# Kernel optimization log

Hardware: AMD Instinct MI355X
Metric: run time of the kernel (lower is better)

## Reference

```python
import jax, jax.numpy as jnp
import numpy as np
from itertools import product

GRID_N = 256
N_RAYS, N_SAMPLES = 2048, 128


def setup_inputs() -> dict:
    key = jax.random.key(0)
    k1, k2 = jax.random.split(key)
    sdf_grid = jax.random.normal(k1, (GRID_N, GRID_N, GRID_N), dtype=jnp.float32)
    # monotone voxel-center coordinates over [-1, 1] (sdf_util.get_grid_pts analog)
    x_grid = jnp.linspace(-1.0, 1.0, GRID_N, dtype=jnp.float32)
    y_grid = jnp.linspace(-1.0, 1.0, GRID_N, dtype=jnp.float32)
    z_grid = jnp.linspace(-1.0, 1.0, GRID_N, dtype=jnp.float32)
    # single object pose (sdf_map_pose); identity as in SDFModel.__init__
    pose = jnp.eye(4, dtype=jnp.float32)
    # query sample points in [-0.95, 0.95]^3
    pts = jax.random.uniform(k2, (N_RAYS, N_SAMPLES, 3), dtype=jnp.float32,
                             minval=-0.95, maxval=0.95)
    return {"sdf_grid": sdf_grid, "x_grid": x_grid, "y_grid": y_grid,
            "z_grid": z_grid, "pose": pose, "pts": pts}


def _interp_axis(p, x):
    """Per-dim bucketize + left/right distances (torch.bucketize right=False
    == searchsorted side='left'). p: [N] sorted, x: [K]. Returns idx_l, idx_r,
    dist_l, dist_r, overall, all shape [K]."""
    n = p.shape[0]
    idx_r = jnp.searchsorted(p, x, side="left")
    idx_r = jnp.where(idx_r >= n, n - 1, idx_r)
    idx_l = jnp.clip(idx_r - 1, 0, n - 1)
    dist_l = jnp.maximum(x - p[idx_l], 0.0)
    dist_r = jnp.maximum(p[idx_r] - x, 0.0)
    both_zero = (dist_l == 0.0) & (dist_r == 0.0)
    dist_l = jnp.where(both_zero, 1.0, dist_l)
    dist_r = jnp.where(both_zero, 1.0, dist_r)
    return idx_l, idx_r, dist_l, dist_r, dist_l + dist_r


def reference(sdf_grid, x_grid, y_grid, z_grid, pose, pts):
    # SDFModel.transform with a single pose: x_obj = T_inv @ [x; 1]
    x = pts.reshape(-1, 3)                               # [K, 3]
    T_inv = jnp.linalg.inv(pose)
    x_obj = x @ T_inv[:3, :3].T + T_inv[:3, 3]           # [K, 3]

    grids = (x_grid, y_grid, z_grid)
    axis_data = [_interp_axis(p, x_obj[:, d]) for d, p in enumerate(grids)]
    idxs = [(a[0], a[1]) for a in axis_data]
    dists = [(a[2], a[3]) for a in axis_data]
    overalls = jnp.stack([a[4] for a in axis_data])      # [3, K]

    numerator = jnp.zeros(x.shape[0], dtype=sdf_grid.dtype)
    for indexer in product([0, 1], repeat=3):            # 8 corners
        ix, iy, iz = (idx[onoff] for onoff, idx in zip(indexer, idxs))
        w = (dists[0][1 - indexer[0]] * dists[1][1 - indexer[1]]
             * dists[2][1 - indexer[2]])                  # opposite-side weights
        numerator = numerator + sdf_grid[ix, iy, iz] * w
    denominator = jnp.prod(overalls, axis=0)             # [K]
    return numerator / denominator                       # [K] squeezed SDF
```

## Files before the change

### kernel.cpp

```cpp
#include <hip/hip_runtime.h>

#define GRID_N 256

typedef float float2u __attribute__((ext_vector_type(2), aligned(4)));

__global__ void pose_invert_kernel(const float* __restrict__ pose,
                                   float* __restrict__ tinv) {
    if (threadIdx.x != 0 || blockIdx.x != 0) return;
    float a[4][8];
    for (int i = 0; i < 4; ++i)
        for (int j = 0; j < 4; ++j) {
            a[i][j]     = pose[i * 4 + j];
            a[i][j + 4] = (i == j) ? 1.0f : 0.0f;
        }
    for (int c = 0; c < 4; ++c) {
        int piv = c;
        float best = fabsf(a[c][c]);
        for (int r = c + 1; r < 4; ++r) {
            float v = fabsf(a[r][c]);
            if (v > best) { best = v; piv = r; }
        }
        if (piv != c)
            for (int j = 0; j < 8; ++j) {
                float t = a[c][j]; a[c][j] = a[piv][j]; a[piv][j] = t;
            }
        float inv = 1.0f / a[c][c];
        for (int j = 0; j < 8; ++j) a[c][j] *= inv;
        for (int r = 0; r < 4; ++r) {
            if (r == c) continue;
            float f = a[r][c];
            for (int j = 0; j < 8; ++j) a[r][j] -= f * a[c][j];
        }
    }
    for (int i = 0; i < 3; ++i)
        for (int j = 0; j < 4; ++j)
            tinv[i * 4 + j] = a[i][j + 4];
}

__global__ __launch_bounds__(256) void sdf_interp_kernel(
    const float* __restrict__ sdf,
    const float* __restrict__ xg,
    const float* __restrict__ yg,
    const float* __restrict__ zg,
    const float* __restrict__ tinv,
    const float* __restrict__ pts,
    float* __restrict__ out,
    int K) {
    __shared__ float sx[GRID_N];
    __shared__ float sy[GRID_N];
    __shared__ float sz[GRID_N];
    sx[threadIdx.x] = xg[threadIdx.x];
    sy[threadIdx.x] = yg[threadIdx.x];
    sz[threadIdx.x] = zg[threadIdx.x];
    __syncthreads();

    const int i = blockIdx.x * blockDim.x + threadIdx.x;
    if (i >= K) return;

    const float px = pts[3 * i + 0];
    const float py = pts[3 * i + 1];
    const float pz = pts[3 * i + 2];
    const float x = tinv[0] * px + tinv[1] * py + tinv[2]  * pz + tinv[3];
    const float y = tinv[4] * px + tinv[5] * py + tinv[6]  * pz + tinv[7];
    const float z = tinv[8] * px + tinv[9] * py + tinv[10] * pz + tinv[11];

#define FIND(P, V, L, R)                                                  \
    int L, R;                                                             \
    {                                                                     \
        const float p0 = P[0];                                            \
        const float invh = 1.0f / (P[1] - p0);                            \
        int r = (int)ceilf(((V) - p0) * invh);                            \
        r = (r < 0) ? 0 : ((r > GRID_N - 1) ? GRID_N - 1 : r);            \
        while (r > 0 && P[r - 1] >= (V)) --r;                             \
        while (r < GRID_N - 1 && P[r] < (V)) ++r;                         \
        R = r;                                                            \
        L = (r > 0) ? r - 1 : 0;                                          \
    }

    FIND(sx, x, ixl, ixr)
    FIND(sy, y, iyl, iyr)
    FIND(sz, z, izl, izr)
#undef FIND

    const int bx0 = ixl * (GRID_N * GRID_N);
    const int bx1 = ixr * (GRID_N * GRID_N);
    const int by0 = iyl * GRID_N;
    const int by1 = iyr * GRID_N;

    const float2u z00 = *(const float2u*)(sdf + bx0 + by0 + izl);
    const float2u z01 = *(const float2u*)(sdf + bx0 + by1 + izl);
    const float2u z10 = *(const float2u*)(sdf + bx1 + by0 + izl);
    const float2u z11 = *(const float2u*)(sdf + bx1 + by1 + izl);

    float dlx = fmaxf(x - sx[ixl], 0.0f);
    float drx = fmaxf(sx[ixr] - x, 0.0f);
    if (dlx == 0.0f && drx == 0.0f) { dlx = 1.0f; drx = 1.0f; }
    float dly = fmaxf(y - sy[iyl], 0.0f);
    float dry = fmaxf(sy[iyr] - y, 0.0f);
    if (dly == 0.0f && dry == 0.0f) { dly = 1.0f; dry = 1.0f; }
    float dlz = fmaxf(z - sz[izl], 0.0f);
    float drz = fmaxf(sz[izr] - z, 0.0f);
    if (dlz == 0.0f && drz == 0.0f) { dlz = 1.0f; drz = 1.0f; }

    const bool zsame = (izr == izl);
    const float v000 = z00.x, v001 = zsame ? z00.x : z00.y;
    const float v010 = z01.x, v011 = zsame ? z01.x : z01.y;
    const float v100 = z10.x, v101 = zsame ? z10.x : z10.y;
    const float v110 = z11.x, v111 = zsame ? z11.x : z11.y;

    const float numer =
        drx * (dry * (v000 * drz + v001 * dlz) +
               dly * (v010 * drz + v011 * dlz)) +
        dlx * (dry * (v100 * drz + v101 * dlz) +
               dly * (v110 * drz + v111 * dlz));

    const float denom = (dlx + drx) * (dly + dry) * (dlz + drz);
    out[i] = numer / denom;
}

extern "C" void kernel_launch(void* const* d_in, const int* in_sizes, int n_in,
                              void* d_out, int out_size, void* d_ws, size_t ws_size,
                              hipStream_t stream) {
    const float* sdf  = (const float*)d_in[0];
    const float* xg   = (const float*)d_in[1];
    const float* yg   = (const float*)d_in[2];
    const float* zg   = (const float*)d_in[3];
    const float* pose = (const float*)d_in[4];
    const float* pts  = (const float*)d_in[5];
    float* out = (float*)d_out;
    float* tinv = (float*)d_ws;

    const int K = in_sizes[5] / 3;

    pose_invert_kernel<<<1, 64, 0, stream>>>(pose, tinv);

    const int block = 256;
    const int grid = (K + block - 1) / block;
    sdf_interp_kernel<<<grid, block, 0, stream>>>(sdf, xg, yg, zg, tinv, pts,
                                                  out, K);
}
```

Baseline: 31.57 us.

## Fuse pose inversion into interp kernel and process two points per thread

Drops the separate single-thread pose-inversion launch. Each block now inverts the pose itself in thread 0 into shared memory, which removes one kernel launch and the dependency between the two kernels. Each thread now handles two sample points and issues all eight corner gathers before computing either result, which is meant to expose more memory-level parallelism. The gathers also use nontemporal loads. The trade-offs are a redundant serial inversion in every block, half as many blocks, and higher register pressure.

Result: faster. 25.79 us (median of 2 runs) (-18.3%).

```diff
diff --git a/kernel.cpp b/kernel.cpp
--- a/kernel.cpp
+++ b/kernel.cpp
@@ -4,65 +4,57 @@
 
 typedef float float2u __attribute__((ext_vector_type(2), aligned(4)));
 
-__global__ void pose_invert_kernel(const float* __restrict__ pose,
-                                   float* __restrict__ tinv) {
-    if (threadIdx.x != 0 || blockIdx.x != 0) return;
-    float a[4][8];
-    for (int i = 0; i < 4; ++i)
-        for (int j = 0; j < 4; ++j) {
-            a[i][j]     = pose[i * 4 + j];
-            a[i][j + 4] = (i == j) ? 1.0f : 0.0f;
-        }
-    for (int c = 0; c < 4; ++c) {
-        int piv = c;
-        float best = fabsf(a[c][c]);
-        for (int r = c + 1; r < 4; ++r) {
-            float v = fabsf(a[r][c]);
-            if (v > best) { best = v; piv = r; }
-        }
-        if (piv != c)
-            for (int j = 0; j < 8; ++j) {
-                float t = a[c][j]; a[c][j] = a[piv][j]; a[piv][j] = t;
-            }
-        float inv = 1.0f / a[c][c];
-        for (int j = 0; j < 8; ++j) a[c][j] *= inv;
-        for (int r = 0; r < 4; ++r) {
-            if (r == c) continue;
-            float f = a[r][c];
-            for (int j = 0; j < 8; ++j) a[r][j] -= f * a[c][j];
-        }
-    }
-    for (int i = 0; i < 3; ++i)
-        for (int j = 0; j < 4; ++j)
-            tinv[i * 4 + j] = a[i][j + 4];
-}
-
 __global__ __launch_bounds__(256) void sdf_interp_kernel(
     const float* __restrict__ sdf,
     const float* __restrict__ xg,
     const float* __restrict__ yg,
     const float* __restrict__ zg,
-    const float* __restrict__ tinv,
+    const float* __restrict__ pose,
     const float* __restrict__ pts,
     float* __restrict__ out,
     int K) {
     __shared__ float sx[GRID_N];
     __shared__ float sy[GRID_N];
     __shared__ float sz[GRID_N];
+    __shared__ float ti[12];
+
+    if (threadIdx.x == 0) {
+        float a[4][8];
+        for (int r = 0; r < 4; ++r)
+            for (int c = 0; c < 4; ++c) {
+                a[r][c]     = pose[r * 4 + c];
+                a[r][c + 4] = (r == c) ? 1.0f : 0.0f;
+            }
+        for (int c = 0; c < 4; ++c) {
+            int piv = c;
+            float best = fabsf(a[c][c]);
+            for (int r = c + 1; r < 4; ++r) {
+                float v = fabsf(a[r][c]);
+                if (v > best) { best = v; piv = r; }
+            }
+            if (piv != c)
+                for (int j = 0; j < 8; ++j) {
+                    float t = a[c][j]; a[c][j] = a[piv][j]; a[piv][j] = t;
+                }
+            float inv = 1.0f / a[c][c];
+            for (int j = 0; j < 8; ++j) a[c][j] *= inv;
+            for (int r = 0; r < 4; ++r) {
+                if (r == c) continue;
+                float f = a[r][c];
+                for (int j = 0; j < 8; ++j) a[r][j] -= f * a[c][j];
+            }
+        }
+        for (int r = 0; r < 3; ++r)
+            for (int c = 0; c < 4; ++c)
+                ti[r * 4 + c] = a[r][c + 4];
+    }
     sx[threadIdx.x] = xg[threadIdx.x];
     sy[threadIdx.x] = yg[threadIdx.x];
     sz[threadIdx.x] = zg[threadIdx.x];
     __syncthreads();
 
-    const int i = blockIdx.x * blockDim.x + threadIdx.x;
-    if (i >= K) return;
-
-    const float px = pts[3 * i + 0];
-    const float py = pts[3 * i + 1];
-    const float pz = pts[3 * i + 2];
-    const float x = tinv[0] * px + tinv[1] * py + tinv[2]  * pz + tinv[3];
-    const float y = tinv[4] * px + tinv[5] * py + tinv[6]  * pz + tinv[7];
-    const float z = tinv[8] * px + tinv[9] * py + tinv[10] * pz + tinv[11];
+    const int i0 = blockIdx.x * (blockDim.x * 2) + threadIdx.x;
+    const int i1 = i0 + 256;
 
 #define FIND(P, V, L, R)                                                  \
     int L, R;                                                             \
@@ -77,45 +69,94 @@
         L = (r > 0) ? r - 1 : 0;                                          \
     }
 
-    FIND(sx, x, ixl, ixr)
-    FIND(sy, y, iyl, iyr)
-    FIND(sz, z, izl, izr)
+#define WEIGHTS(P, V, IL, IR, DL, DR)                                     \
+    float DL = fmaxf((V) - P[IL], 0.0f);                                  \
+    float DR = fmaxf(P[IR] - (V), 0.0f);                                  \
+    if (DL == 0.0f && DR == 0.0f) { DL = 1.0f; DR = 1.0f; }
+
+    float xA, yA, zA;
+    int ixlA, ixrA, iylA, iyrA, izlA, izrA;
+    float2u a00, a01, a10, a11;
+    if (i0 < K) {
+        const float px = pts[3 * i0 + 0];
+        const float py = pts[3 * i0 + 1];
+        const float pz = pts[3 * i0 + 2];
+        xA = ti[0] * px + ti[1] * py + ti[2]  * pz + ti[3];
+        yA = ti[4] * px + ti[5] * py + ti[6]  * pz + ti[7];
+        zA = ti[8] * px + ti[9] * py + ti[10] * pz + ti[11];
+        FIND(sx, xA, l0, r0) ixlA = l0; ixrA = r0;
+        FIND(sy, yA, l1, r1) iylA = l1; iyrA = r1;
+        FIND(sz, zA, l2, r2) izlA = l2; izrA = r2;
+        const int bx0 = ixlA * (GRID_N * GRID_N);
+        const int bx1 = ixrA * (GRID_N * GRID_N);
+        const int by0 = iylA * GRID_N;
+        const int by1 = iyrA * GRID_N;
+        a00 = __builtin_nontemporal_load((const float2u*)(sdf + bx0 + by0 + izlA));
+        a01 = __builtin_nontemporal_load((const float2u*)(sdf + bx0 + by1 + izlA));
+        a10 = __builtin_nontemporal_load((const float2u*)(sdf + bx1 + by0 + izlA));
+        a11 = __builtin_nontemporal_load((const float2u*)(sdf + bx1 + by1 + izlA));
+    }
+
+    float xB, yB, zB;
+    int ixlB, ixrB, iylB, iyrB, izlB, izrB;
+    float2u b00, b01, b10, b11;
+    if (i1 < K) {
+        const float px = pts[3 * i1 + 0];
+        const float py = pts[3 * i1 + 1];
+        const float pz = pts[3 * i1 + 2];
+        xB = ti[0] * px + ti[1] * py + ti[2]  * pz + ti[3];
+        yB = ti[4] * px + ti[5] * py + ti[6]  * pz + ti[7];
+        zB = ti[8] * px + ti[9] * py + ti[10] * pz + ti[11];
+        FIND(sx, xB, l0, r0) ixlB = l0; ixrB = r0;
+        FIND(sy, yB, l1, r1) iylB = l1; iyrB = r1;
+        FIND(sz, zB, l2, r2) izlB = l2; izrB = r2;
+        const int bx0 = ixlB * (GRID_N * GRID_N);
+        const int bx1 = ixrB * (GRID_N * GRID_N);
+        const int by0 = iylB * GRID_N;
+        const int by1 = iyrB * GRID_N;
+        b00 = __builtin_nontemporal_load((const float2u*)(sdf + bx0 + by0 + izlB));
+        b01 = __builtin_nontemporal_load((const float2u*)(sdf + bx0 + by1 + izlB));
+        b10 = __builtin_nontemporal_load((const float2u*)(sdf + bx1 + by0 + izlB));
+        b11 = __builtin_nontemporal_load((const float2u*)(sdf + bx1 + by1 + izlB));
+    }
+
+    if (i0 < K) {
+        WEIGHTS(sx, xA, ixlA, ixrA, dlx, drx)
+        WEIGHTS(sy, yA, iylA, iyrA, dly, dry)
+        WEIGHTS(sz, zA, izlA, izrA, dlz, drz)
+        const bool zs = (izrA == izlA);
+        const float v000 = a00.x, v001 = zs ? a00.x : a00.y;
+        const float v010 = a01.x, v011 = zs ? a01.x : a01.y;
+        const float v100 = a10.x, v101 = zs ? a10.x : a10.y;
+        const float v110 = a11.x, v111 = zs ? a11.x : a11.y;
+        const float numer =
+            drx * (dry * (v000 * drz + v001 * dlz) +
+                   dly * (v010 * drz + v011 * dlz)) +
+            dlx * (dry * (v100 * drz + v101 * dlz) +
+                   dly * (v110 * drz + v111 * dlz));
+        const float denom = (dlx + drx) * (dly + dry) * (dlz + drz);
+        out[i0] = numer / denom;
+    }
+
+    if (i1 < K) {
+        WEIGHTS(sx, xB, ixlB, ixrB, dlx, drx)
+        WEIGHTS(sy, yB, iylB, iyrB, dly, dry)
+        WEIGHTS(sz, zB, izlB, izrB, dlz, drz)
+        const bool zs = (izrB == izlB);
+        const float v000 = b00.x, v001 = zs ? b00.x : b00.y;
+        const float v010 = b01.x, v011 = zs ? b01.x : b01.y;
+        const float v100 = b10.x, v101 = zs ? b10.x : b10.y;
+        const float v110 = b11.x, v111 = zs ? b11.x : b11.y;
+        const float numer =
+            drx * (dry * (v000 * drz + v001 * dlz) +
+                   dly * (v010 * drz + v011 * dlz)) +
+            dlx * (dry * (v100 * drz + v101 * dlz) +
+                   dly * (v110 * drz + v111 * dlz));
+        const float denom = (dlx + drx) * (dly + dry) * (dlz + drz);
+        out[i1] = numer / denom;
+    }
 #undef FIND
-
-    const int bx0 = ixl * (GRID_N * GRID_N);
-    const int bx1 = ixr * (GRID_N * GRID_N);
-    const int by0 = iyl * GRID_N;
-    const int by1 = iyr * GRID_N;
-
-    const float2u z00 = *(const float2u*)(sdf + bx0 + by0 + izl);
-    const float2u z01 = *(const float2u*)(sdf + bx0 + by1 + izl);
-    const float2u z10 = *(const float2u*)(sdf + bx1 + by0 + izl);
-    const float2u z11 = *(const float2u*)(sdf + bx1 + by1 + izl);
-
-    float dlx = fmaxf(x - sx[ixl], 0.0f);
-    float drx = fmaxf(sx[ixr] - x, 0.0f);
-    if (dlx == 0.0f && drx == 0.0f) { dlx = 1.0f; drx = 1.0f; }
-    float dly = fmaxf(y - sy[iyl], 0.0f);
-    float dry = fmaxf(sy[iyr] - y, 0.0f);
-    if (dly == 0.0f && dry == 0.0f) { dly = 1.0f; dry = 1.0f; }
-    float dlz = fmaxf(z - sz[izl], 0.0f);
-    float drz = fmaxf(sz[izr] - z, 0.0f);
-    if (dlz == 0.0f && drz == 0.0f) { dlz = 1.0f; drz = 1.0f; }
-
-    const bool zsame = (izr == izl);
-    const float v000 = z00.x, v001 = zsame ? z00.x : z00.y;
-    const float v010 = z01.x, v011 = zsame ? z01.x : z01.y;
-    const float v100 = z10.x, v101 = zsame ? z10.x : z10.y;
-    const float v110 = z11.x, v111 = zsame ? z11.x : z11.y;
-
-    const float numer =
-        drx * (dry * (v000 * drz + v001 * dlz) +
-               dly * (v010 * drz + v011 * dlz)) +
-        dlx * (dry * (v100 * drz + v101 * dlz) +
-               dly * (v110 * drz + v111 * dlz));
-
-    const float denom = (dlx + drx) * (dly + dry) * (dlz + drz);
-    out[i] = numer / denom;
+#undef WEIGHTS
 }
 
 extern "C" void kernel_launch(void* const* d_in, const int* in_sizes, int n_in,
@@ -128,14 +169,11 @@
     const float* pose = (const float*)d_in[4];
     const float* pts  = (const float*)d_in[5];
     float* out = (float*)d_out;
-    float* tinv = (float*)d_ws;
 
     const int K = in_sizes[5] / 3;
 
-    pose_invert_kernel<<<1, 64, 0, stream>>>(pose, tinv);
-
     const int block = 256;
-    const int grid = (K + block - 1) / block;
-    sdf_interp_kernel<<<grid, block, 0, stream>>>(sdf, xg, yg, zg, tinv, pts,
+    const int grid = (K + block * 2 - 1) / (block * 2);
+    sdf_interp_kernel<<<grid, block, 0, stream>>>(sdf, xg, yg, zg, pose, pts,
                                                   out, K);
 }
```
